# Kernel optimization log

Hardware: AMD Instinct MI355X
Metric: run time of the kernel (lower is better)

The kernel has to match this reference:

```python
import jax, jax.numpy as jnp
import numpy as np

LN_EPS = 1e-5
BOUNDARY_ID = 0  # boundary_ids = {space_id} = {0}


def setup_inputs() -> dict:
    key = jax.random.key(0)
    k1, k2, k3 = jax.random.split(key, 3)
    B, T, D = 16, 8192, 256
    x = jax.random.normal(k1, (B, T, D), dtype=jnp.float32)
    input_ids = jax.random.randint(k2, (B, T), 0, 8, dtype=jnp.int64)
    W_proj = jax.random.normal(k3, (D, D), dtype=jnp.float32) / np.sqrt(D)
    b_proj = jnp.zeros((D,), dtype=jnp.float32)
    gamma = jnp.ones((D,), dtype=jnp.float32)
    beta = jnp.zeros((D,), dtype=jnp.float32)
    return {"x": x, "input_ids": input_ids, "W_proj": W_proj,
            "b_proj": b_proj, "gamma": gamma, "beta": beta}


def _pool(x, input_ids):
    # Boundary-defined segment mean pooling, vectorized via segment_sum.
    B, T, D = x.shape
    boundary = input_ids == BOUNDARY_ID                       # [B,T]
    nonb = ~boundary
    # A segment starts at a non-boundary token at t=0 or right after a boundary.
    prev_is_b = jnp.concatenate(
        [jnp.ones((B, 1), dtype=bool), boundary[:, :-1]], axis=1)
    start = nonb & prev_is_b
    seg = jnp.cumsum(start.astype(jnp.int32), axis=1) - 1     # seg idx per token
    MAXW = T  # static upper bound on number of segments (jit-safe padding)
    row_off = jnp.arange(B, dtype=jnp.int32)[:, None] * MAXW
    dump = B * MAXW  # boundary tokens go to a dummy segment, dropped below
    flat_ids = jnp.where(nonb, seg + row_off, dump).reshape(-1)
    sums = jax.ops.segment_sum(x.reshape(-1, D), flat_ids,
                               num_segments=B * MAXW + 1)[:-1]
    counts = jax.ops.segment_sum(jnp.ones((B * T,), x.dtype), flat_ids,
                                 num_segments=B * MAXW + 1)[:-1]
    sums = sums.reshape(B, MAXW, D)
    counts = counts.reshape(B, MAXW)
    mask = (counts > 0).astype(x.dtype)                       # [B,MAXW]
    padded = sums / jnp.maximum(counts, 1.0)[..., None]       # zeros where empty
    return padded, mask


def reference(x, input_ids, W_proj, b_proj, gamma, beta):
    padded, mask = _pool(x, input_ids)
    out = jnp.einsum('bwd,ed->bwe', padded, W_proj) + b_proj  # nn.Linear
    mu = jnp.mean(out, axis=-1, keepdims=True)
    var = jnp.mean(jnp.square(out - mu), axis=-1, keepdims=True)
    out = (out - mu) * jax.lax.rsqrt(var + LN_EPS) * gamma + beta
    return out, mask
```

## Files before the change

kernel.cpp:

```cpp
#include <hip/hip_runtime.h>
#include <hip/hip_bf16.h>
#include <math.h>

#define BB 16
#define TT 8192
#define DD 256
#define MAXSEG 4096
#define RPB 16
#define LN_EPS 1e-5f

__device__ inline float4 f4add(float4 a, float4 b) {
    a.x += b.x; a.y += b.y; a.z += b.z; a.w += b.w; return a;
}

__global__ __launch_bounds__(256) void prelude(const float* __restrict__ W,
                                               const float* __restrict__ bp,
                                               const float* __restrict__ gamma,
                                               const float* __restrict__ beta,
                                               float* __restrict__ Wt,
                                               float* __restrict__ ln_empty) {
    __shared__ float s1[256];
    __shared__ float s2[256];
    int e = threadIdx.x;
    if (blockIdx.x < DD) {
        int d = blockIdx.x;
        Wt[d * DD + e] = W[e * DD + d];
        return;
    }
    float v = bp[e];
    s1[e] = v;
    s2[e] = v * v;
    __syncthreads();
    for (int o = 128; o > 0; o >>= 1) {
        if (e < o) { s1[e] += s1[e + o]; s2[e] += s2[e + o]; }
        __syncthreads();
    }
    float mu = s1[0] / (float)DD;
    float var = s2[0] / (float)DD - mu * mu;
    float rs = rsqrtf(fmaxf(var, 0.f) + LN_EPS);
    ln_empty[e] = (v - mu) * rs * gamma[e] + beta[e];
}

__global__ __launch_bounds__(1024) void seg_scan(const int* __restrict__ ids,
                                                 int* __restrict__ counts,
                                                 int* __restrict__ seg_start,
                                                 int* __restrict__ nseg_g,
                                                 float* __restrict__ mask_out) {
    const int TPT = 8;
    __shared__ int wtot_s[16];
    __shared__ int wtot_n[16];
    __shared__ int segs[MAXSEG];
    __shared__ int pvals[MAXSEG];

    int b = blockIdx.x;
    int tid = threadIdx.x;
    int lane = tid & 63;
    int wv = tid >> 6;
    const int* row = ids + b * TT;
    int t0 = tid * TPT;

    int4 q0 = ((const int4*)(row + t0))[0];
    int4 q1 = ((const int4*)(row + t0))[1];
    int v[TPT] = {q0.x, q0.y, q0.z, q0.w, q1.x, q1.y, q1.z, q1.w};
    int prev = (tid == 0) ? 0 : row[t0 - 1];

    bool nb[TPT], st[TPT];
    int cstart = 0, cnon = 0;
#pragma unroll
    for (int j = 0; j < TPT; ++j) {
        nb[j] = (v[j] != 0);
        int pv = (j == 0) ? prev : v[j - 1];
        st[j] = nb[j] && (pv == 0);
        cstart += st[j] ? 1 : 0;
        cnon += nb[j] ? 1 : 0;
    }

    int ss = cstart, sn = cnon;
#pragma unroll
    for (int o = 1; o < 64; o <<= 1) {
        int us = __shfl_up(ss, o);
        int un = __shfl_up(sn, o);
        if (lane >= o) { ss += us; sn += un; }
    }
    if (lane == 63) { wtot_s[wv] = ss; wtot_n[wv] = sn; }
    __syncthreads();

    int bs = 0, bn = 0, tot_s = 0, tot_n = 0;
#pragma unroll
    for (int j = 0; j < 16; ++j) {
        int a = wtot_s[j], c = wtot_n[j];
        if (j < wv) { bs += a; bn += c; }
        tot_s += a; tot_n += c;
    }
    bs += ss - cstart;
    bn += sn - cnon;

#pragma unroll
    for (int j = 0; j < TPT; ++j) {
        if (st[j]) { segs[bs] = t0 + j; pvals[bs] = bn; bs++; }
        bn += nb[j] ? 1 : 0;
    }
    __syncthreads();

    int ns = tot_s;
    for (int w = tid; w < TT; w += 1024) {
        int c = 0;
        if (w < ns) {
            int pe = (w + 1 < ns) ? pvals[w + 1] : tot_n;
            c = pe - pvals[w];
            seg_start[b * TT + w] = segs[w];
        }
        counts[b * TT + w] = c;
        mask_out[b * TT + w] = (w < ns) ? 1.0f : 0.0f;
    }
    if (tid == 0) nseg_g[b] = ns;
}

__global__ __launch_bounds__(256) void pool_gemm_ln(
    const float* __restrict__ x, const float* __restrict__ Wt,
    const float* __restrict__ bp, const float* __restrict__ gamma,
    const float* __restrict__ beta, const int* __restrict__ counts,
    const int* __restrict__ seg_start, const int* __restrict__ nseg,
    const float* __restrict__ ln_e, float* __restrict__ out) {
    __shared__ float pooled[RPB][DD];
    __shared__ float mu_s[RPB];
    __shared__ float rs_s[RPB];

    int b = blockIdx.y;
    int wbase = blockIdx.x * RPB;
    int ns = nseg[b];
    int e = threadIdx.x;
    int lane = e & 63;
    int wv = e >> 6;

    if (wbase >= ns) {
        float v = ln_e[e];
#pragma unroll
        for (int r = 0; r < RPB; ++r)
            out[((size_t)(b * TT + wbase + r)) * DD + e] = v;
        return;
    }
    int nr = min(RPB, ns - wbase);

    for (int r = wv; r < nr; r += 4) {
        int w = wbase + r;
        int s = seg_start[b * TT + w];
        int len = counts[b * TT + w];
        const float4* xp = (const float4*)(x + ((size_t)(b * TT + s)) * DD) + lane;
        float4 a0 = {0, 0, 0, 0}, a1 = a0, a2 = a0, a3 = a0;
        int t = 0;
        for (; t + 4 <= len; t += 4) {
            float4 v0 = xp[(t + 0) * 64];
            float4 v1 = xp[(t + 1) * 64];
            float4 v2 = xp[(t + 2) * 64];
            float4 v3 = xp[(t + 3) * 64];
            a0 = f4add(a0, v0); a1 = f4add(a1, v1);
            a2 = f4add(a2, v2); a3 = f4add(a3, v3);
        }
        for (; t < len; ++t) a0 = f4add(a0, xp[t * 64]);
        a0 = f4add(f4add(a0, a1), f4add(a2, a3));
        float inv = 1.f / (float)len;
        a0.x *= inv; a0.y *= inv; a0.z *= inv; a0.w *= inv;
        *(float4*)&pooled[r][lane * 4] = a0;
    }
    __syncthreads();

    float acc[RPB];
    float bias = bp[e];
#pragma unroll
    for (int r = 0; r < RPB; ++r) acc[r] = bias;

    for (int d0 = 0; d0 < DD; d0 += 4) {
        float w0 = Wt[(d0 + 0) * DD + e];
        float w1 = Wt[(d0 + 1) * DD + e];
        float w2 = Wt[(d0 + 2) * DD + e];
        float w3 = Wt[(d0 + 3) * DD + e];
#pragma unroll
        for (int r = 0; r < RPB; ++r) {
            const float4 p = *(const float4*)&pooled[r][d0];
            acc[r] = fmaf(p.x, w0, acc[r]);
            acc[r] = fmaf(p.y, w1, acc[r]);
            acc[r] = fmaf(p.z, w2, acc[r]);
            acc[r] = fmaf(p.w, w3, acc[r]);
        }
    }
    __syncthreads();

#pragma unroll
    for (int r = 0; r < RPB; ++r) pooled[r][e] = acc[r];
    __syncthreads();

    for (int r = wv; r < nr; r += 4) {
        float s = 0.f, sq = 0.f;
#pragma unroll
        for (int j = 0; j < 4; ++j) {
            float v = pooled[r][lane + j * 64];
            s += v;
            sq += v * v;
        }
#pragma unroll
        for (int o = 32; o > 0; o >>= 1) {
            s += __shfl_down(s, o);
            sq += __shfl_down(sq, o);
        }
        if (lane == 0) {
            float mu = s / (float)DD;
            float var = sq / (float)DD - mu * mu;
            mu_s[r] = mu;
            rs_s[r] = rsqrtf(fmaxf(var, 0.f) + LN_EPS);
        }
    }
    __syncthreads();

    float ga = gamma[e], be = beta[e], lev = ln_e[e];
    for (int r = 0; r < RPB; ++r) {
        float v;
        if (r < nr)
            v = (pooled[r][e] - mu_s[r]) * rs_s[r] * ga + be;
        else
            v = lev;
        out[((size_t)(b * TT + wbase + r)) * DD + e] = v;
    }
}

extern "C" void kernel_launch(void* const* d_in, const int* in_sizes, int n_in,
                              void* d_out, int out_size, void* d_ws, size_t ws_size,
                              hipStream_t stream) {
    const float* x = (const float*)d_in[0];
    const int* ids = (const int*)d_in[1];
    const float* W = (const float*)d_in[2];
    const float* bp = (const float*)d_in[3];
    const float* gamma = (const float*)d_in[4];
    const float* beta = (const float*)d_in[5];

    float* out = (float*)d_out;
    float* mask = out + (size_t)BB * TT * DD;

    char* ws = (char*)d_ws;
    int* counts = (int*)ws;
    int* seg_start = (int*)(ws + (size_t)BB * TT * 4);
    int* nseg = (int*)(ws + (size_t)2 * BB * TT * 4);
    float* Wt = (float*)(ws + (size_t)2 * BB * TT * 4 + 256);
    float* ln_e = Wt + DD * DD;

    hipLaunchKernelGGL(prelude, dim3(DD + 1), dim3(DD), 0, stream,
                       W, bp, gamma, beta, Wt, ln_e);
    hipLaunchKernelGGL(seg_scan, dim3(BB), dim3(1024), 0, stream,
                       ids, counts, seg_start, nseg, mask);
    hipLaunchKernelGGL(pool_gemm_ln, dim3(TT / RPB, BB), dim3(256), 0, stream,
                       x, Wt, bp, gamma, beta, counts, seg_start, nseg, ln_e, out);
}
```

Baseline: 295.5 us.

## Give each wave private rows in pool-GEMM-LN, drop block barriers

The fused pool/GEMM/LayerNorm kernel now has each wavefront own 4 output rows end to end. The wave pools them into shared memory, computes a 4x4-per-lane register tile of the projection with float4 weight loads, and does LayerNorm with wave shuffles and float4 stores. This removes all __syncthreads and the shared-memory round trip for the GEMM result, and lets waves with no valid rows skip the GEMM. The grid is also transposed so batch is the fast dimension, which spreads busy and empty tiles more evenly across blocks. Each wave now loads the full Wt on its own, so weight traffic from L2/L1 goes up.

```diff
diff --git a/kernel.cpp b/kernel.cpp
--- a/kernel.cpp
+++ b/kernel.cpp
@@ -123,103 +123,114 @@
     const int* __restrict__ seg_start, const int* __restrict__ nseg,
     const float* __restrict__ ln_e, float* __restrict__ out) {
     __shared__ float pooled[RPB][DD];
-    __shared__ float mu_s[RPB];
-    __shared__ float rs_s[RPB];
-
-    int b = blockIdx.y;
-    int wbase = blockIdx.x * RPB;
+
+    int b = blockIdx.x;
+    int wbase = blockIdx.y * RPB;
     int ns = nseg[b];
-    int e = threadIdx.x;
-    int lane = e & 63;
-    int wv = e >> 6;
+    int tid = threadIdx.x;
+    int lane = tid & 63;
+    int wv = tid >> 6;
+    int r0 = wv * 4;
+    size_t outbase = ((size_t)(b * TT + wbase)) * DD + 4 * lane;
 
     if (wbase >= ns) {
-        float v = ln_e[e];
-#pragma unroll
-        for (int r = 0; r < RPB; ++r)
-            out[((size_t)(b * TT + wbase + r)) * DD + e] = v;
+        float4 lv = *(const float4*)(ln_e + 4 * lane);
+#pragma unroll
+        for (int r = 0; r < 4; ++r)
+            *(float4*)(out + outbase + (size_t)(r0 + r) * DD) = lv;
         return;
     }
     int nr = min(RPB, ns - wbase);
 
-    for (int r = wv; r < nr; r += 4) {
-        int w = wbase + r;
-        int s = seg_start[b * TT + w];
-        int len = counts[b * TT + w];
-        const float4* xp = (const float4*)(x + ((size_t)(b * TT + s)) * DD) + lane;
-        float4 a0 = {0, 0, 0, 0}, a1 = a0, a2 = a0, a3 = a0;
-        int t = 0;
-        for (; t + 4 <= len; t += 4) {
-            float4 v0 = xp[(t + 0) * 64];
-            float4 v1 = xp[(t + 1) * 64];
-            float4 v2 = xp[(t + 2) * 64];
-            float4 v3 = xp[(t + 3) * 64];
-            a0 = f4add(a0, v0); a1 = f4add(a1, v1);
-            a2 = f4add(a2, v2); a3 = f4add(a3, v3);
-        }
-        for (; t < len; ++t) a0 = f4add(a0, xp[t * 64]);
-        a0 = f4add(f4add(a0, a1), f4add(a2, a3));
-        float inv = 1.f / (float)len;
-        a0.x *= inv; a0.y *= inv; a0.z *= inv; a0.w *= inv;
-        *(float4*)&pooled[r][lane * 4] = a0;
-    }
-    __syncthreads();
-
-    float acc[RPB];
-    float bias = bp[e];
-#pragma unroll
-    for (int r = 0; r < RPB; ++r) acc[r] = bias;
-
-    for (int d0 = 0; d0 < DD; d0 += 4) {
-        float w0 = Wt[(d0 + 0) * DD + e];
-        float w1 = Wt[(d0 + 1) * DD + e];
-        float w2 = Wt[(d0 + 2) * DD + e];
-        float w3 = Wt[(d0 + 3) * DD + e];
-#pragma unroll
-        for (int r = 0; r < RPB; ++r) {
-            const float4 p = *(const float4*)&pooled[r][d0];
-            acc[r] = fmaf(p.x, w0, acc[r]);
-            acc[r] = fmaf(p.y, w1, acc[r]);
-            acc[r] = fmaf(p.z, w2, acc[r]);
-            acc[r] = fmaf(p.w, w3, acc[r]);
-        }
-    }
-    __syncthreads();
-
-#pragma unroll
-    for (int r = 0; r < RPB; ++r) pooled[r][e] = acc[r];
-    __syncthreads();
-
-    for (int r = wv; r < nr; r += 4) {
-        float s = 0.f, sq = 0.f;
-#pragma unroll
-        for (int j = 0; j < 4; ++j) {
-            float v = pooled[r][lane + j * 64];
-            s += v;
-            sq += v * v;
-        }
-#pragma unroll
-        for (int o = 32; o > 0; o >>= 1) {
-            s += __shfl_down(s, o);
-            sq += __shfl_down(sq, o);
-        }
-        if (lane == 0) {
-            float mu = s / (float)DD;
-            float var = sq / (float)DD - mu * mu;
-            mu_s[r] = mu;
-            rs_s[r] = rsqrtf(fmaxf(var, 0.f) + LN_EPS);
-        }
-    }
-    __syncthreads();
-
-    float ga = gamma[e], be = beta[e], lev = ln_e[e];
-    for (int r = 0; r < RPB; ++r) {
-        float v;
-        if (r < nr)
-            v = (pooled[r][e] - mu_s[r]) * rs_s[r] * ga + be;
-        else
-            v = lev;
-        out[((size_t)(b * TT + wbase + r)) * DD + e] = v;
+#pragma unroll
+    for (int r = 0; r < 4; ++r) {
+        int row = r0 + r;
+        if (row < nr) {
+            int w = wbase + row;
+            int s = seg_start[b * TT + w];
+            int len = counts[b * TT + w];
+            const float4* xp = (const float4*)(x + ((size_t)(b * TT + s)) * DD) + lane;
+            float4 a0 = {0, 0, 0, 0}, a1 = a0, a2 = a0, a3 = a0;
+            int t = 0;
+            for (; t + 4 <= len; t += 4) {
+                a0 = f4add(a0, xp[(t + 0) * 64]);
+                a1 = f4add(a1, xp[(t + 1) * 64]);
+                a2 = f4add(a2, xp[(t + 2) * 64]);
+                a3 = f4add(a3, xp[(t + 3) * 64]);
+            }
+            for (; t < len; ++t) a0 = f4add(a0, xp[t * 64]);
+            a0 = f4add(f4add(a0, a1), f4add(a2, a3));
+            float inv = 1.f / (float)len;
+            a0.x *= inv; a0.y *= inv; a0.z *= inv; a0.w *= inv;
+            *(float4*)&pooled[row][lane * 4] = a0;
+        }
+    }
+
+    float4 acc[4];
+    float4 bias4 = *(const float4*)(bp + 4 * lane);
+#pragma unroll
+    for (int r = 0; r < 4; ++r) acc[r] = bias4;
+
+    if (r0 < nr) {
+        const float4* WtR = (const float4*)Wt;
+#pragma unroll 2
+        for (int d0 = 0; d0 < DD; d0 += 4) {
+            float4 w0 = WtR[(d0 + 0) * 64 + lane];
+            float4 w1 = WtR[(d0 + 1) * 64 + lane];
+            float4 w2 = WtR[(d0 + 2) * 64 + lane];
+            float4 w3 = WtR[(d0 + 3) * 64 + lane];
+#pragma unroll
+            for (int r = 0; r < 4; ++r) {
+                const float4 p = *(const float4*)&pooled[r0 + r][d0];
+                acc[r].x = fmaf(p.x, w0.x, acc[r].x);
+                acc[r].y = fmaf(p.x, w0.y, acc[r].y);
+                acc[r].z = fmaf(p.x, w0.z, acc[r].z);
+                acc[r].w = fmaf(p.x, w0.w, acc[r].w);
+                acc[r].x = fmaf(p.y, w1.x, acc[r].x);
+                acc[r].y = fmaf(p.y, w1.y, acc[r].y);
+                acc[r].z = fmaf(p.y, w1.z, acc[r].z);
+                acc[r].w = fmaf(p.y, w1.w, acc[r].w);
+                acc[r].x = fmaf(p.z, w2.x, acc[r].x);
+                acc[r].y = fmaf(p.z, w2.y, acc[r].y);
+                acc[r].z = fmaf(p.z, w2.z, acc[r].z);
+                acc[r].w = fmaf(p.z, w2.w, acc[r].w);
+                acc[r].x = fmaf(p.w, w3.x, acc[r].x);
+                acc[r].y = fmaf(p.w, w3.y, acc[r].y);
+                acc[r].z = fmaf(p.w, w3.z, acc[r].z);
+                acc[r].w = fmaf(p.w, w3.w, acc[r].w);
+            }
+        }
+    }
+
+    float4 ga4 = *(const float4*)(gamma + 4 * lane);
+    float4 be4 = *(const float4*)(beta + 4 * lane);
+    float4 lv = *(const float4*)(ln_e + 4 * lane);
+#pragma unroll
+    for (int r = 0; r < 4; ++r) {
+        int row = r0 + r;
+        float4 v;
+        if (row < nr) {
+            float s = acc[r].x + acc[r].y + acc[r].z + acc[r].w;
+            float sq = acc[r].x * acc[r].x + acc[r].y * acc[r].y +
+                       acc[r].z * acc[r].z + acc[r].w * acc[r].w;
+#pragma unroll
+            for (int o = 32; o > 0; o >>= 1) {
+                s += __shfl_down(s, o);
+                sq += __shfl_down(sq, o);
+            }
+            s = __shfl(s, 0);
+            sq = __shfl(sq, 0);
+            float mu = s * (1.f / (float)DD);
+            float var = sq * (1.f / (float)DD) - mu * mu;
+            float rs = rsqrtf(fmaxf(var, 0.f) + LN_EPS);
+            v.x = (acc[r].x - mu) * rs * ga4.x + be4.x;
+            v.y = (acc[r].y - mu) * rs * ga4.y + be4.y;
+            v.z = (acc[r].z - mu) * rs * ga4.z + be4.z;
+            v.w = (acc[r].w - mu) * rs * ga4.w + be4.w;
+        } else {
+            v = lv;
+        }
+        *(float4*)(out + outbase + (size_t)row * DD) = v;
     }
 }
 
@@ -247,6 +258,6 @@
                        W, bp, gamma, beta, Wt, ln_e);
     hipLaunchKernelGGL(seg_scan, dim3(BB), dim3(1024), 0, stream,
                        ids, counts, seg_start, nseg, mask);
-    hipLaunchKernelGGL(pool_gemm_ln, dim3(TT / RPB, BB), dim3(256), 0, stream,
+    hipLaunchKernelGGL(pool_gemm_ln, dim3(BB, TT / RPB), dim3(256), 0, stream,
                        x, Wt, bp, gamma, beta, counts, seg_start, nseg, ln_e, out);
 }
```

Result: faster. 285.9 us (-3.2%).
